# Kernel optimization log

Measured on AMD Instinct MI355X. Metric: run time of the kernel, lower is better.

The kernel has to match this reference:

```python
import jax, jax.numpy as jnp
import numpy as np

B, T = 64, 500
NUM_CONCEPT, DIM, SIZE_MEM = 1024, 64, 50


def setup_inputs() -> dict:
    key = jax.random.key(0)
    ks = jax.random.split(key, 16)
    d = DIM

    def lin(k, fin, fout):
        k1, k2 = jax.random.split(k)
        s = 1.0 / np.sqrt(fin)
        return (jax.random.uniform(k1, (fin, fout), jnp.float32, -s, s),
                jax.random.uniform(k2, (fout,), jnp.float32, -s, s))

    Wf, bf = lin(ks[4], 2 * d, d)
    We, be = lin(ks[5], d, d)
    Wa, ba = lin(ks[6], d, d)
    Wab, bab = lin(ks[7], d, 1)
    Wd, bd = lin(ks[8], d, 1)
    return {
        'concept_seq': jax.random.randint(ks[0], (B, T), 0, NUM_CONCEPT),
        'correct_seq': jax.random.randint(ks[1], (B, T), 0, 2),
        'num_concept': NUM_CONCEPT,
        'embed_key': jax.random.normal(ks[2], (NUM_CONCEPT, d), jnp.float32),
        'embed_value': jax.random.normal(ks[3], (2 * NUM_CONCEPT, d), jnp.float32),
        'Mk': jax.random.normal(ks[9], (SIZE_MEM, d), jnp.float32) * np.sqrt(2.0 / d),
        'Mv0': jax.random.normal(ks[10], (SIZE_MEM, d), jnp.float32) * np.sqrt(2.0 / d),
        'Wf': Wf, 'bf': bf, 'We': We, 'be': be, 'Wa': Wa, 'ba': ba,
        'Wab': Wab, 'bab': bab, 'Wd': Wd, 'bd': bd,
    }


def _forward(concept_seq, correct_seq, num_concept, embed_key, embed_value,
             Mk, Mv0, Wf, bf, We, be, Wa, ba, Wab, bab, Wd, bd):
    x = concept_seq + num_concept * correct_seq          # [B,T]
    k = embed_key[concept_seq]                           # [B,T,d]
    v = embed_value[x]                                   # [B,T,d]
    w = jax.nn.softmax(jnp.einsum('btd,sd->bts', k, Mk), axis=-1)  # [B,T,S]
    e = jax.nn.sigmoid(v @ We + be)                      # [B,T,d]
    a = jnp.tanh(v @ Wa + ba)                            # [B,T,d]

    bsz = concept_seq.shape[0]
    Mv_init = jnp.broadcast_to(Mv0, (bsz,) + Mv0.shape)  # [B,S,d]

    def step(Mvt, inp):
        wt, et, at = inp                                 # [B,S],[B,d],[B,d]
        u = wt[:, :, None]
        Mv_new = Mvt * (1.0 - u * et[:, None, :]) + u * at[:, None, :]
        return Mv_new, Mvt                               # emit pre-update state

    wT = jnp.swapaxes(w, 0, 1)                           # [T,B,S]
    eT = jnp.swapaxes(e, 0, 1)
    aT = jnp.swapaxes(a, 0, 1)
    _, Mv_pre = jax.lax.scan(step, Mv_init, (wT, eT, aT))  # [T,B,S,d]

    r = jnp.einsum('tbs,tbsd->btd', wT, Mv_pre)          # read content [B,T,d]
    f = jnp.tanh(jnp.concatenate([r, k], axis=-1) @ Wf + bf)
    stu_ability = jnp.tanh(f @ Wab + bab)                # [B,T,1] (dropout = eval identity)
    que_diff = jnp.tanh(k @ Wd + bd)                     # [B,T,1]
    return jax.nn.sigmoid(3.0 * stu_ability - que_diff)[..., 0]  # [B,T]


def reference(concept_seq, correct_seq, num_concept, embed_key, embed_value,
              Mk, Mv0, Wf, bf, We, be, Wa, ba, Wab, bab, Wd, bd):
    return _forward(concept_seq, correct_seq, num_concept, embed_key, embed_value,
                    Mk, Mv0, Wf, bf, We, be, Wa, ba, Wab, bab, Wd, bd)
```

## Files before the change

### kernel.cpp

```cpp
#include <hip/hip_runtime.h>
#include <hip/hip_bf16.h>
#include <math.h>

#define BB 64
#define TT 500
#define DD 64
#define SS 50
#define PP 10
#define LL 50

typedef float v2f __attribute__((ext_vector_type(2)));

__device__ __forceinline__ float sigmoidf_(float x) { return 1.0f / (1.0f + __expf(-x)); }

__global__ __launch_bounds__(64) void k1_tables(
    const float* __restrict__ embed_key,
    const float* __restrict__ embed_value,
    const float* __restrict__ Mk,
    const float* __restrict__ We, const float* __restrict__ be,
    const float* __restrict__ Wa, const float* __restrict__ ba,
    int ncon, int nv,
    float* __restrict__ wTab, float* __restrict__ eaTab)
{
    const int lane = threadIdx.x;
    if ((int)blockIdx.x < ncon) {
        const int c = blockIdx.x;
        __shared__ float mkS[SS][DD + 1];
        __shared__ float kS[DD];
        kS[lane] = embed_key[c * DD + lane];
        for (int s = 0; s < SS; ++s)
            mkS[s][lane] = Mk[s * DD + lane];
        __syncthreads();

        float sc = -1e30f;
        if (lane < SS) {
            float acc = 0.f;
            #pragma unroll
            for (int dd = 0; dd < DD; ++dd)
                acc = fmaf(kS[dd], mkS[lane][dd], acc);
            sc = acc;
        }
        float m = sc;
        #pragma unroll
        for (int off = 32; off >= 1; off >>= 1)
            m = fmaxf(m, __shfl_xor(m, off));
        float ex = (lane < SS) ? __expf(sc - m) : 0.f;
        float ssum = ex;
        #pragma unroll
        for (int off = 32; off >= 1; off >>= 1)
            ssum += __shfl_xor(ssum, off);
        if (lane < SS)
            wTab[c * SS + lane] = ex / ssum;
    } else {
        const int x = blockIdx.x - ncon;
        __shared__ float vS[DD];
        vS[lane] = embed_value[x * DD + lane];
        __syncthreads();
        float acc_e = be[lane];
        float acc_a = ba[lane];
        #pragma unroll
        for (int i = 0; i < DD; ++i) {
            const float vi = vS[i];
            acc_e = fmaf(vi, We[i * DD + lane], acc_e);
            acc_a = fmaf(vi, Wa[i * DD + lane], acc_a);
        }
        float2 ea;
        ea.x = sigmoidf_(acc_e);
        ea.y = tanhf(acc_a);
        *(float2*)&eaTab[((size_t)x * DD + lane) * 2] = ea;
    }
}


#define SCAN_STAGE()                                                          \
    const int b = blockIdx.x / PP, p = blockIdx.x % PP;                       \
    const int tid = threadIdx.x;                                              \
    const int lane = tid & 63, sg = tid >> 6;                                 \
    const int t0g = p * LL;                                                   \
    if (tid < LL) {                                                           \
        const int c = cseq[b * TT + t0g + tid];                               \
        cL[tid] = c;                                                          \
        xL[tid] = c + ncp[0] * corr[b * TT + t0g + tid];                      \
    }                                                                         \
    __syncthreads();                                                          \
    for (int i = tid; i < LL * 64; i += 256) {                                \
        const int t = i >> 6, l = i & 63;                                     \
        const int sg_ = l >> 4, j_ = l & 15;                                  \
        const int st_ = (SS * sg_) >> 2, en_ = (SS * (sg_ + 1)) >> 2;         \
        const int s_ = st_ + j_;                                              \
        wLds[t][l] = (s_ < en_) ? wTab[cL[t] * SS + s_] : 0.f;                \
        eaLds[t][l] = *(const float2*)&eaTab[((size_t)xL[t] * DD + l) * 2];   \
    }

#define LOADW(t)                                                              \
    const float4 wv0 = *(const float4*)&wLds[t][sg * 16];                     \
    const float4 wv1 = *(const float4*)&wLds[t][sg * 16 + 4];                 \
    const float4 wv2 = *(const float4*)&wLds[t][sg * 16 + 8];                 \
    const v2f w6 = *(const v2f*)&wLds[t][sg * 16 + 12];                       \
    const v2f w[7] = {{wv0.x, wv0.y}, {wv0.z, wv0.w}, {wv1.x, wv1.y},         \
                      {wv1.z, wv1.w}, {wv2.x, wv2.y}, {wv2.z, wv2.w}, w6};

__global__ __launch_bounds__(256) void k2a_maps(
    const int* __restrict__ cseq, const int* __restrict__ corr,
    const int* __restrict__ ncp,
    const float* __restrict__ wTab, const float* __restrict__ eaTab,
    float* __restrict__ Aout, float* __restrict__ Bout)
{
    __shared__ int cL[LL], xL[LL];
    __shared__ float __align__(16) wLds[LL][64];
    __shared__ float2 __align__(8) eaLds[LL][64];

    SCAN_STAGE()
    __syncthreads();

    v2f A[7], Bc[7];
    #pragma unroll
    for (int j = 0; j < 7; ++j) { A[j] = (v2f){1.f, 1.f}; Bc[j] = (v2f){0.f, 0.f}; }

    const v2f one2 = {1.f, 1.f};
    #pragma unroll 2
    for (int t = 0; t < LL; ++t) {
        LOADW(t)
        const float2 ea = eaLds[t][lane];
        const v2f e2 = {ea.x, ea.x}, a2 = {ea.y, ea.y};
        #pragma unroll
        for (int j = 0; j < 7; ++j) {
            const v2f al = __builtin_elementwise_fma(-w[j], e2, one2);
            const v2f be = w[j] * a2;
            A[j]  = al * A[j];
            Bc[j] = __builtin_elementwise_fma(al, Bc[j], be);
        }
    }

    const int st = (SS * sg) >> 2, en = (SS * (sg + 1)) >> 2;
    float* Ap = Aout + (size_t)blockIdx.x * SS * DD;
    float* Bp = Bout + (size_t)blockIdx.x * SS * DD;
    #pragma unroll
    for (int j = 0; j < 6; ++j) {
        const int s0 = st + 2 * j;
        Ap[(size_t)s0 * DD + lane] = A[j].x;
        Ap[(size_t)(s0 + 1) * DD + lane] = A[j].y;
        Bp[(size_t)s0 * DD + lane] = Bc[j].x;
        Bp[(size_t)(s0 + 1) * DD + lane] = Bc[j].y;
    }
    if (st + 12 < en) {
        Ap[(size_t)(st + 12) * DD + lane] = A[6].x;
        Bp[(size_t)(st + 12) * DD + lane] = Bc[6].x;
    }
}

__global__ __launch_bounds__(256) void k2b_combine(
    const float* __restrict__ Mv0,
    float* __restrict__ Aio, const float* __restrict__ Bin)
{
    const int gid = blockIdx.x * 256 + threadIdx.x;
    const int d = gid & 63;
    const int s = (gid >> 6) % SS;
    const int b = gid / (SS * 64);
    float m = Mv0[s * DD + d];
    #pragma unroll
    for (int p = 0; p < PP; ++p) {
        const size_t o = (((size_t)(b * PP + p)) * SS + s) * DD + d;
        const float a = Aio[o], bb = Bin[o];
        m = fmaf(a, m, bb);
        Aio[o] = m;
    }
}

__global__ __launch_bounds__(256) void k2c_replay(
    const int* __restrict__ cseq, const int* __restrict__ corr,
    const int* __restrict__ ncp,
    const float* __restrict__ wTab, const float* __restrict__ eaTab,
    const float* __restrict__ Mv0, const float* __restrict__ Mst,
    float* __restrict__ rOut)
{
    __shared__ int cL[LL], xL[LL];
    __shared__ float __align__(16) wLds[LL][64];
    __shared__ float2 __align__(8) eaLds[LL][64];
    __shared__ float parts[10][4][DD];

    SCAN_STAGE()

    const int st = (SS * sg) >> 2, en = (SS * (sg + 1)) >> 2;
    const float* msrc = (p == 0) ? Mv0
                       : (Mst + (size_t)(b * PP + p - 1) * SS * DD);
    v2f m[7];
    #pragma unroll
    for (int j = 0; j < 7; ++j) {
        const int s0 = st + 2 * j, s1 = s0 + 1;
        v2f mm = {0.f, 0.f};
        if (s0 < en) mm.x = msrc[(size_t)s0 * DD + lane];
        if (s1 < en) mm.y = msrc[(size_t)s1 * DD + lane];
        m[j] = mm;
    }
    __syncthreads();

    float* rb = rOut + ((size_t)b * TT + p * LL) * DD;
    for (int tq = 0; tq < LL / 10; ++tq) {
        #pragma unroll
        for (int u = 0; u < 10; ++u) {
            const int t = tq * 10 + u;
            LOADW(t)
            const float2 ea = eaLds[t][lane];
            const v2f e2 = {ea.x, ea.x}, na2 = {-ea.y, -ea.y};
            v2f r2 = {0.f, 0.f};
            #pragma unroll
            for (int j = 0; j < 7; ++j) {
                const v2f mv = m[j];
                r2 = __builtin_elementwise_fma(w[j], mv, r2);
                const v2f g = __builtin_elementwise_fma(e2, mv, na2);
                m[j] = __builtin_elementwise_fma(-w[j], g, mv);
            }
            parts[u][sg][lane] = r2.x + r2.y;
        }
        __syncthreads();
        for (int o = tid; o < 10 * DD; o += 256) {
            const int u2 = o >> 6, d2 = o & 63;
            rb[(size_t)(tq * 10 + u2) * DD + d2] =
                parts[u2][0][d2] + parts[u2][1][d2]
              + parts[u2][2][d2] + parts[u2][3][d2];
        }
        __syncthreads();
    }
}

__global__ __launch_bounds__(256) void k3_output(
    const int* __restrict__ cseq,
    const float* __restrict__ embed_key,
    const float* __restrict__ rOut,
    const float* __restrict__ Wf, const float* __restrict__ bf,
    const float* __restrict__ Wab, const float* __restrict__ bab,
    const float* __restrict__ Wd, const float* __restrict__ bd,
    float* __restrict__ out)
{
    const int tid = threadIdx.x;
    const int tx = tid & 15, ty = tid >> 4;
    const int bt0 = blockIdx.x * 64;

    __shared__ float __align__(16) wfS[128][64];
    __shared__ float __align__(16) catT[128][68];
    __shared__ float qS[64];
    __shared__ float wdS[64];
    __shared__ float redS[64][17];

    #pragma unroll
    for (int k = 0; k < 8; ++k) {
        const int idx = tid + k * 256;
        ((float4*)wfS)[idx] = ((const float4*)Wf)[idx];
    }
    if (tid < 64) wdS[tid] = Wd[tid];

    {
        const int d = tid & 63;
        const int g = tid >> 6;
        #pragma unroll
        for (int mq = 0; mq < 16; ++mq) {
            const int btl = g + 4 * mq;
            const int bt = bt0 + btl;
            const int c = cseq[bt];
            catT[d][btl] = rOut[(size_t)bt * DD + d];
            catT[64 + d][btl] = embed_key[c * DD + d];
        }
    }
    __syncthreads();

    if (tid < 64) {
        const int btl = tid;
        float q = 0.f;
        #pragma unroll
        for (int i = 0; i < DD; ++i)
            q = fmaf(catT[64 + i][btl], wdS[i], q);
        qS[btl] = q;
    }

    float acc[4][4] = {{0.f}};
    #pragma unroll 8
    for (int i = 0; i < 128; ++i) {
        const float4 wf = *(const float4*)&wfS[i][tx * 4];
        const float4 ct = *(const float4*)&catT[i][ty * 4];
        acc[0][0] = fmaf(ct.x, wf.x, acc[0][0]);
        acc[0][1] = fmaf(ct.x, wf.y, acc[0][1]);
        acc[0][2] = fmaf(ct.x, wf.z, acc[0][2]);
        acc[0][3] = fmaf(ct.x, wf.w, acc[0][3]);
        acc[1][0] = fmaf(ct.y, wf.x, acc[1][0]);
        acc[1][1] = fmaf(ct.y, wf.y, acc[1][1]);
        acc[1][2] = fmaf(ct.y, wf.z, acc[1][2]);
        acc[1][3] = fmaf(ct.y, wf.w, acc[1][3]);
        acc[2][0] = fmaf(ct.z, wf.x, acc[2][0]);
        acc[2][1] = fmaf(ct.z, wf.y, acc[2][1]);
        acc[2][2] = fmaf(ct.z, wf.z, acc[2][2]);
        acc[2][3] = fmaf(ct.z, wf.w, acc[2][3]);
        acc[3][0] = fmaf(ct.w, wf.x, acc[3][0]);
        acc[3][1] = fmaf(ct.w, wf.y, acc[3][1]);
        acc[3][2] = fmaf(ct.w, wf.z, acc[3][2]);
        acc[3][3] = fmaf(ct.w, wf.w, acc[3][3]);
    }

    #pragma unroll
    for (int ii = 0; ii < 4; ++ii) {
        float pacc = 0.f;
        #pragma unroll
        for (int jj = 0; jj < 4; ++jj) {
            const int j = tx * 4 + jj;
            const float f = tanhf(acc[ii][jj] + bf[j]);
            pacc = fmaf(f, Wab[j], pacc);
        }
        redS[ty * 4 + ii][tx] = pacc;
    }
    __syncthreads();

    if (tid < 64) {
        const int btl = tid;
        float s = 0.f;
        #pragma unroll
        for (int t2 = 0; t2 < 16; ++t2)
            s += redS[btl][t2];
        const float stu  = tanhf(s + bab[0]);
        const float diff = tanhf(qS[btl] + bd[0]);
        out[bt0 + btl] = sigmoidf_(3.0f * stu - diff);
    }
}

extern "C" void kernel_launch(void* const* d_in, const int* in_sizes, int n_in,
                              void* d_out, int out_size, void* d_ws, size_t ws_size,
                              hipStream_t stream)
{
    const int*   concept_seq = (const int*)  d_in[0];
    const int*   correct_seq = (const int*)  d_in[1];
    const int*   num_concept = (const int*)  d_in[2];
    const float* embed_key   = (const float*)d_in[3];
    const float* embed_value = (const float*)d_in[4];
    const float* Mk          = (const float*)d_in[5];
    const float* Mv0         = (const float*)d_in[6];
    const float* Wf          = (const float*)d_in[7];
    const float* bf          = (const float*)d_in[8];
    const float* We          = (const float*)d_in[9];
    const float* be          = (const float*)d_in[10];
    const float* Wa          = (const float*)d_in[11];
    const float* ba          = (const float*)d_in[12];
    const float* Wab         = (const float*)d_in[13];
    const float* bab         = (const float*)d_in[14];
    const float* Wd          = (const float*)d_in[15];
    const float* bd          = (const float*)d_in[16];
    float* out = (float*)d_out;

    const int NCON = in_sizes[3] / DD;
    const int NV   = in_sizes[4] / DD;

    float* wTab  = (float*)d_ws;
    float* eaTab = wTab + (size_t)NCON * SS;
    float* Abuf  = eaTab + (size_t)NV * DD * 2;
    float* Bbuf  = Abuf + (size_t)BB * PP * SS * DD;
    float* rOut  = Bbuf + (size_t)BB * PP * SS * DD;

    k1_tables<<<NCON + NV, 64, 0, stream>>>(
        embed_key, embed_value, Mk, We, be, Wa, ba,
        NCON, NV, wTab, eaTab);

    k2a_maps<<<BB * PP, 256, 0, stream>>>(
        concept_seq, correct_seq, num_concept,
        wTab, eaTab, Abuf, Bbuf);

    k2b_combine<<<(BB * SS * DD) / 256, 256, 0, stream>>>(
        Mv0, Abuf, Bbuf);

    k2c_replay<<<BB * PP, 256, 0, stream>>>(
        concept_seq, correct_seq, num_concept,
        wTab, eaTab, Mv0, Abuf, rOut);

    k3_output<<<(BB * TT) / 64, 256, 0, stream>>>(
        concept_seq, embed_key, rOut,
        Wf, bf, Wab, bab, Wd, bd, out);
}
```

Before: 152.6 us.

## Fuse chunk-prefix combine, replay and output head into one kernel

Removes the separate combine and output kernels. Each replay block now rebuilds its chunk's starting memory by applying all earlier chunks' affine maps itself, which replaces the sequential combine pass. It then keeps the read vectors in shared memory and computes the Wf/tanh/ability/difficulty head in place, so the rOut round trip and two launches disappear. The cost is redundant prefix work that grows with chunk index (up to 9 extra A/B passes) and a slower per-wave scalar matvec head instead of the tiled GEMM.

```diff
diff --git a/kernel.cpp b/kernel.cpp
--- a/kernel.cpp
+++ b/kernel.cpp
@@ -149,53 +149,55 @@
     }
 }
 
-__global__ __launch_bounds__(256) void k2b_combine(
-    const float* __restrict__ Mv0,
-    float* __restrict__ Aio, const float* __restrict__ Bin)
-{
-    const int gid = blockIdx.x * 256 + threadIdx.x;
-    const int d = gid & 63;
-    const int s = (gid >> 6) % SS;
-    const int b = gid / (SS * 64);
-    float m = Mv0[s * DD + d];
-    #pragma unroll
-    for (int p = 0; p < PP; ++p) {
-        const size_t o = (((size_t)(b * PP + p)) * SS + s) * DD + d;
-        const float a = Aio[o], bb = Bin[o];
-        m = fmaf(a, m, bb);
-        Aio[o] = m;
-    }
-}
-
-__global__ __launch_bounds__(256) void k2c_replay(
+__global__ __launch_bounds__(256) void k2_fused(
     const int* __restrict__ cseq, const int* __restrict__ corr,
     const int* __restrict__ ncp,
     const float* __restrict__ wTab, const float* __restrict__ eaTab,
-    const float* __restrict__ Mv0, const float* __restrict__ Mst,
-    float* __restrict__ rOut)
+    const float* __restrict__ Mv0,
+    const float* __restrict__ Abuf, const float* __restrict__ Bbuf,
+    const float* __restrict__ embed_key,
+    const float* __restrict__ Wf, const float* __restrict__ bf,
+    const float* __restrict__ Wab, const float* __restrict__ bab,
+    const float* __restrict__ Wd, const float* __restrict__ bd,
+    float* __restrict__ out)
 {
     __shared__ int cL[LL], xL[LL];
-    __shared__ float __align__(16) wLds[LL][64];
-    __shared__ float2 __align__(8) eaLds[LL][64];
-    __shared__ float parts[10][4][DD];
+    __shared__ __align__(16) char smemRaw[61440];
+    float  (*wLds)[64]     = (float (*)[64])(smemRaw);
+    float2 (*eaLds)[64]    = (float2 (*)[64])(smemRaw + 12800);
+    float  (*parts)[4][64] = (float (*)[4][64])(smemRaw + 38400);
+    float  (*rL)[64]       = (float (*)[64])(smemRaw + 48640);
+    float  (*wfS)[64]      = (float (*)[64])(smemRaw);
+    float  (*kS)[64]       = (float (*)[64])(smemRaw + 32768);
 
     SCAN_STAGE()
 
     const int st = (SS * sg) >> 2, en = (SS * (sg + 1)) >> 2;
-    const float* msrc = (p == 0) ? Mv0
-                       : (Mst + (size_t)(b * PP + p - 1) * SS * DD);
     v2f m[7];
     #pragma unroll
     for (int j = 0; j < 7; ++j) {
         const int s0 = st + 2 * j, s1 = s0 + 1;
         v2f mm = {0.f, 0.f};
-        if (s0 < en) mm.x = msrc[(size_t)s0 * DD + lane];
-        if (s1 < en) mm.y = msrc[(size_t)s1 * DD + lane];
+        if (s0 < en) mm.x = Mv0[(size_t)s0 * DD + lane];
+        if (s1 < en) mm.y = Mv0[(size_t)s1 * DD + lane];
         m[j] = mm;
     }
+    for (int q = 0; q < p; ++q) {
+        const float* Aq = Abuf + (size_t)(b * PP + q) * SS * DD;
+        const float* Bq = Bbuf + (size_t)(b * PP + q) * SS * DD;
+        #pragma unroll
+        for (int j = 0; j < 7; ++j) {
+            const int s0 = st + 2 * j, s1 = s0 + 1;
+            if (s0 < en)
+                m[j].x = fmaf(Aq[(size_t)s0 * DD + lane], m[j].x,
+                              Bq[(size_t)s0 * DD + lane]);
+            if (s1 < en)
+                m[j].y = fmaf(Aq[(size_t)s1 * DD + lane], m[j].y,
+                              Bq[(size_t)s1 * DD + lane]);
+        }
+    }
     __syncthreads();
 
-    float* rb = rOut + ((size_t)b * TT + p * LL) * DD;
     for (int tq = 0; tq < LL / 10; ++tq) {
         #pragma unroll
         for (int u = 0; u < 10; ++u) {
@@ -216,108 +218,54 @@
         __syncthreads();
         for (int o = tid; o < 10 * DD; o += 256) {
             const int u2 = o >> 6, d2 = o & 63;
-            rb[(size_t)(tq * 10 + u2) * DD + d2] =
-                parts[u2][0][d2] + parts[u2][1][d2]
-              + parts[u2][2][d2] + parts[u2][3][d2];
+            rL[tq * 10 + u2][d2] = parts[u2][0][d2] + parts[u2][1][d2]
+                                 + parts[u2][2][d2] + parts[u2][3][d2];
         }
         __syncthreads();
     }
-}
-
-__global__ __launch_bounds__(256) void k3_output(
-    const int* __restrict__ cseq,
-    const float* __restrict__ embed_key,
-    const float* __restrict__ rOut,
-    const float* __restrict__ Wf, const float* __restrict__ bf,
-    const float* __restrict__ Wab, const float* __restrict__ bab,
-    const float* __restrict__ Wd, const float* __restrict__ bd,
-    float* __restrict__ out)
-{
-    const int tid = threadIdx.x;
-    const int tx = tid & 15, ty = tid >> 4;
-    const int bt0 = blockIdx.x * 64;
-
-    __shared__ float __align__(16) wfS[128][64];
-    __shared__ float __align__(16) catT[128][68];
-    __shared__ float qS[64];
-    __shared__ float wdS[64];
-    __shared__ float redS[64][17];
 
     #pragma unroll
-    for (int k = 0; k < 8; ++k) {
-        const int idx = tid + k * 256;
+    for (int k8 = 0; k8 < 8; ++k8) {
+        const int idx = tid + k8 * 256;
         ((float4*)wfS)[idx] = ((const float4*)Wf)[idx];
     }
-    if (tid < 64) wdS[tid] = Wd[tid];
-
-    {
-        const int d = tid & 63;
-        const int g = tid >> 6;
-        #pragma unroll
-        for (int mq = 0; mq < 16; ++mq) {
-            const int btl = g + 4 * mq;
-            const int bt = bt0 + btl;
-            const int c = cseq[bt];
-            catT[d][btl] = rOut[(size_t)bt * DD + d];
-            catT[64 + d][btl] = embed_key[c * DD + d];
-        }
+    for (int i = tid; i < LL * 64; i += 256) {
+        const int t = i >> 6, d = i & 63;
+        kS[t][d] = embed_key[cL[t] * DD + d];
     }
     __syncthreads();
 
-    if (tid < 64) {
-        const int btl = tid;
-        float q = 0.f;
-        #pragma unroll
-        for (int i = 0; i < DD; ++i)
-            q = fmaf(catT[64 + i][btl], wdS[i], q);
-        qS[btl] = q;
-    }
-
-    float acc[4][4] = {{0.f}};
-    #pragma unroll 8
-    for (int i = 0; i < 128; ++i) {
-        const float4 wf = *(const float4*)&wfS[i][tx * 4];
-        const float4 ct = *(const float4*)&catT[i][ty * 4];
-        acc[0][0] = fmaf(ct.x, wf.x, acc[0][0]);
-        acc[0][1] = fmaf(ct.x, wf.y, acc[0][1]);
-        acc[0][2] = fmaf(ct.x, wf.z, acc[0][2]);
-        acc[0][3] = fmaf(ct.x, wf.w, acc[0][3]);
-        acc[1][0] = fmaf(ct.y, wf.x, acc[1][0]);
-        acc[1][1] = fmaf(ct.y, wf.y, acc[1][1]);
-        acc[1][2] = fmaf(ct.y, wf.z, acc[1][2]);
-        acc[1][3] = fmaf(ct.y, wf.w, acc[1][3]);
-        acc[2][0] = fmaf(ct.z, wf.x, acc[2][0]);
-        acc[2][1] = fmaf(ct.z, wf.y, acc[2][1]);
-        acc[2][2] = fmaf(ct.z, wf.z, acc[2][2]);
-        acc[2][3] = fmaf(ct.z, wf.w, acc[2][3]);
-        acc[3][0] = fmaf(ct.w, wf.x, acc[3][0]);
-        acc[3][1] = fmaf(ct.w, wf.y, acc[3][1]);
-        acc[3][2] = fmaf(ct.w, wf.z, acc[3][2]);
-        acc[3][3] = fmaf(ct.w, wf.w, acc[3][3]);
-    }
-
-    #pragma unroll
-    for (int ii = 0; ii < 4; ++ii) {
-        float pacc = 0.f;
-        #pragma unroll
-        for (int jj = 0; jj < 4; ++jj) {
-            const int j = tx * 4 + jj;
-            const float f = tanhf(acc[ii][jj] + bf[j]);
-            pacc = fmaf(f, Wab[j], pacc);
-        }
-        redS[ty * 4 + ii][tx] = pacc;
-    }
-    __syncthreads();
-
-    if (tid < 64) {
-        const int btl = tid;
-        float s = 0.f;
-        #pragma unroll
-        for (int t2 = 0; t2 < 16; ++t2)
-            s += redS[btl][t2];
-        const float stu  = tanhf(s + bab[0]);
-        const float diff = tanhf(qS[btl] + bd[0]);
-        out[bt0 + btl] = sigmoidf_(3.0f * stu - diff);
+    const int j = lane;
+    const float bf_j = bf[j];
+    const float wab_j = Wab[j];
+    const float wd_j = Wd[j];
+    const float bab0 = bab[0], bd0 = bd[0];
+    float* ob = out + (size_t)b * TT + t0g;
+
+    for (int g8 = 0; g8 < 13; ++g8) {
+        const int t = g8 * 4 + sg;
+        if (t < LL) {
+            float acc = bf_j;
+            #pragma unroll
+            for (int i = 0; i < DD; ++i)
+                acc = fmaf(rL[t][i], wfS[i][j], acc);
+            #pragma unroll
+            for (int i = 0; i < DD; ++i)
+                acc = fmaf(kS[t][i], wfS[DD + i][j], acc);
+            const float f = tanhf(acc);
+            float pv = f * wab_j;
+            float qv = kS[t][j] * wd_j;
+            #pragma unroll
+            for (int off = 32; off >= 1; off >>= 1) {
+                pv += __shfl_xor(pv, off);
+                qv += __shfl_xor(qv, off);
+            }
+            if (j == 0) {
+                const float stu  = tanhf(pv + bab0);
+                const float diff = tanhf(qv + bd0);
+                ob[t] = sigmoidf_(3.0f * stu - diff);
+            }
+        }
     }
 }
 
@@ -351,7 +299,6 @@
     float* eaTab = wTab + (size_t)NCON * SS;
     float* Abuf  = eaTab + (size_t)NV * DD * 2;
     float* Bbuf  = Abuf + (size_t)BB * PP * SS * DD;
-    float* rOut  = Bbuf + (size_t)BB * PP * SS * DD;
 
     k1_tables<<<NCON + NV, 64, 0, stream>>>(
         embed_key, embed_value, Mk, We, be, Wa, ba,
@@ -361,14 +308,8 @@
         concept_seq, correct_seq, num_concept,
         wTab, eaTab, Abuf, Bbuf);
 
-    k2b_combine<<<(BB * SS * DD) / 256, 256, 0, stream>>>(
-        Mv0, Abuf, Bbuf);
-
-    k2c_replay<<<BB * PP, 256, 0, stream>>>(
+    k2_fused<<<BB * PP, 256, 0, stream>>>(
         concept_seq, correct_seq, num_concept,
-        wTab, eaTab, Mv0, Abuf, rOut);
-
-    k3_output<<<(BB * TT) / 64, 256, 0, stream>>>(
-        concept_seq, embed_key, rOut,
-        Wf, bf, Wab, bab, Wd, bd, out);
+        wTab, eaTab, Mv0, Abuf, Bbuf,
+        embed_key, Wf, bf, Wab, bab, Wd, bd, out);
 }
```

After: 224.9 us. 1.47x slower.
